# Performance work log

Measured on AMD Instinct MI355X. Metric: run time of the kernel, lower is better.

The kernel has to match this reference:

```python
import jax, jax.numpy as jnp
import numpy as np

ROW = COL = 8   # unfold tile size
KS = 5          # gaussian raster kernel size
C1 = 6          # high-freq feature split

def conv2d(x, w, b=None, pad=0):
    y = jax.lax.conv_general_dilated(x, w, (1, 1), [(pad, pad), (pad, pad)],
                                     dimension_numbers=('NCHW', 'OIHW', 'NCHW'))
    if b is not None:
        y = y + b[None, :, None, None]
    return y

def unfold_tiles(x, r, c):
    # non-overlapping Unfold(kernel=(r,c), stride=(r,c)) -> [B*L, C, r, c]
    B, C, H, W = x.shape
    x = x.reshape(B, C, H // r, r, W // c, c).transpose(0, 2, 4, 1, 3, 5)
    return x.reshape(B * (H // r) * (W // c), C, r, c)

def fold_tiles(t, B, C, H, W, r, c):
    t = t.reshape(B, H // r, W // c, C, r, c).transpose(0, 3, 1, 4, 2, 5)
    return t.reshape(B, C, H, W)

def setup_inputs() -> dict:
    key = jax.random.key(0)
    ks = jax.random.split(key, 16)
    B, NF, H, W, P = 32, 48, 128, 128, 81
    inp = {
        'ms': jax.random.normal(ks[0], (B, 4, 32, 32), jnp.float32),
        'feat': jax.random.normal(ks[1], (B, NF, H, W), jnp.float32),
        'V': jax.random.normal(ks[2], (B, NF, H, W), jnp.float32),
        'logits_raw': jax.random.normal(ks[3], (B, P, H, W), jnp.float32),
        'sigma_x': jax.random.uniform(ks[4], (P,), jnp.float32, 0.2, 3.0),
        'sigma_y': jax.random.uniform(ks[5], (P,), jnp.float32, 0.2, 3.0),
        'opacity': jax.random.uniform(ks[6], (P,), jnp.float32, 0.1, 1.0),
        'rho': jax.random.uniform(ks[7], (P,), jnp.float32, -0.9, 0.9),
        'w_v2': jax.random.normal(ks[8], (42, 42, 1, 1), jnp.float32) * 0.05,
        'w_fine': jax.random.normal(ks[9], (4, NF, 3, 3), jnp.float32) * 0.05,
        'b_fine': jax.random.normal(ks[10], (4,), jnp.float32) * 0.05,
        'w_res': jax.random.normal(ks[11], (4, NF, 1, 1), jnp.float32) * 0.05,
        'b_res': jax.random.normal(ks[12], (4,), jnp.float32) * 0.05,
    }
    return inp

def reference(ms, feat, V, logits_raw, sigma_x, sigma_y, opacity, rho,
              w_v2, w_fine, b_fine, w_res, b_res):
    B, nf, H, W = feat.shape
    # soft class assignment (gumbel_softmax tau=1, zero-noise deterministic surrogate)
    logits = jax.nn.softmax(logits_raw, axis=1)
    feat1, lr_feat = feat[:, :C1], feat[:, C1:]
    V1, V2 = V[:, :C1], V[:, C1:]
    # H,W are already multiples of ROW/COL -> bicubic-to-same-size is identity
    uf = unfold_tiles(feat1, ROW, COL)        # [B*L, c1, 8, 8]
    ul = unfold_tiles(logits, ROW, COL)       # [B*L, P, 8, 8]
    uv1 = unfold_tiles(V1, ROW, COL)          # [B*L, c1, 8, 8]
    # weighted gaussian params per in-tile position, averaged over all tiles
    pm = ul.reshape(ul.shape[0], ul.shape[1], -1).mean(axis=0)   # [P, 64]
    wsx = sigma_x @ pm; wsy = sigma_y @ pm                       # [64]
    wop = opacity @ pm; wr = rho @ pm                            # [64]
    # 2x2 covariance per point, analytic inverse
    a = wsx ** 2; bcv = wr * wsx * wsy; d = wsy ** 2
    det = a * d - bcv ** 2
    i00 = d / det; i01 = -bcv / det; i11 = a / det
    ax = jnp.linspace(-5.0, 5.0, KS)
    xx = ax[:, None]; yy = ax[None, :]
    z = -0.5 * (i00[:, None, None] * xx ** 2 + 2.0 * i01[:, None, None] * xx * yy
                + i11[:, None, None] * yy ** 2)
    kern = jnp.exp(z) / (2.0 * jnp.pi * jnp.sqrt(det))[:, None, None]   # [64, KS, KS]
    kern = kern / kern.max(axis=(-2, -1), keepdims=True)
    kern = kern * wop[:, None, None]
    # splat: place each point's kernel centered at its grid position in the 8x8 tile
    pad = KS // 2
    ii = jnp.arange(ROW * COL) // COL
    jj = jnp.arange(ROW * COL) % COL
    canvas = jnp.zeros((ROW + 2 * pad, COL + 2 * pad), kern.dtype)
    place = jax.vmap(lambda k, i, j: jax.lax.dynamic_update_slice(canvas, k, (i, j)))
    K = place(kern, ii, jj)[:, pad:pad + ROW, pad:pad + COL]             # [64, 8, 8]
    colors = uf.reshape(uf.shape[0], C1, ROW * COL)                      # [N, c1, 64]
    rendered = jnp.einsum('ncp,phw->nchw', colors, K) * uv1              # modulate by V1
    hr = fold_tiles(rendered, B, C1, H, W, ROW, COL)                     # [B, c1, H, W]
    # squeeze-style channel attention on low branch, modulated by V2
    gap = lr_feat.mean(axis=(2, 3), keepdims=True)
    attn = jax.nn.sigmoid(conv2d(gap, w_v2))
    lr_mod = lr_feat * attn * V2
    out_feat = jnp.concatenate([hr, lr_mod], axis=1)                     # [B, n_feats, H, W]
    up_ms = jax.image.resize(ms, (B, ms.shape[1], H, W), method='bilinear')
    out = conv2d(out_feat, w_fine, b_fine, pad=1) + conv2d(feat, w_res, b_res) + up_ms
    return out
```

## Files before the change

### kernel.cpp

```cpp
#include <hip/hip_runtime.h>

#define NBATCH 32
#define NFEAT 48
#define C1c 6
#define LRC 42
#define HH 128
#define WW 128
#define HWSZ 16384
#define NP 81
#define NQ 64

#define OFF_PM   0
#define OFF_GAP  5184
#define OFF_K    6528
#define OFF_ATTN 10624
#define OFF_WB   11968
#define OFF_HR   14272

__global__ __launch_bounds__(256, 2) void k_phase1(const float* __restrict__ logits,
                                                   const float* __restrict__ feat,
                                                   const float* __restrict__ ms,
                                                   const float* __restrict__ w_res,
                                                   const float* __restrict__ b_fine,
                                                   const float* __restrict__ b_res,
                                                   float* __restrict__ pm_sum,
                                                   float* __restrict__ gap,
                                                   float* __restrict__ out) {
    int bid = blockIdx.x;
    int tid = threadIdx.x;
    if (bid < 512) {
        int b   = bid >> 4;
        int ygp = (bid >> 2) & 3;
        int qq  = bid & 3;
        int x   = tid & 127;
        int yg  = ygp * 2 + (tid >> 7);
        float acc[NP];
#pragma unroll
        for (int p = 0; p < NP; ++p) acc[p] = 0.f;
        for (int k = 0; k < 4; ++k) {
            int y = yg + 8 * (qq * 4 + k);
            const float* base = logits + (size_t)b * NP * HWSZ + (y << 7) + x;
            float ev[NP];
            float s = 0.f;
#pragma unroll
            for (int p = 0; p < NP; ++p) { ev[p] = __expf(base[(size_t)p * HWSZ]); s += ev[p]; }
            float inv = 1.f / s;
#pragma unroll
            for (int p = 0; p < NP; ++p) acc[p] += ev[p] * inv;
        }
        int lane = tid & 63;
#pragma unroll
        for (int p = 0; p < NP; ++p) {
            float e = acc[p];
            e += __shfl_xor(e, 8);
            e += __shfl_xor(e, 16);
            e += __shfl_xor(e, 32);
            if (lane < 8) atomicAdd(&pm_sum[p * NQ + (yg << 3) + lane], e);
        }
    } else {
        int gid = bid - 512;
        int b     = gid >> 3;
        int strip = gid & 7;
        int row = (strip << 4) + (tid >> 4);
        int x0  = (tid & 15) << 3;
        int poff = (row << 7) + x0;
        int lane = tid & 63;
        const float* fb = feat + (((size_t)b * NFEAT) << 14);
        float a[8][4];
#pragma unroll
        for (int j = 0; j < 8; ++j)
#pragma unroll
            for (int o = 0; o < 4; ++o) a[j][o] = 0.f;
        for (int c = 0; c < NFEAT; ++c) {
            const float* fp = fb + ((size_t)c << 14) + poff;
            float4 f0 = *(const float4*)fp;
            float4 f1 = *(const float4*)(fp + 4);
            float wr0 = w_res[c], wr1 = w_res[NFEAT + c], wr2 = w_res[2 * NFEAT + c], wr3 = w_res[3 * NFEAT + c];
            float px[8] = { f0.x, f0.y, f0.z, f0.w, f1.x, f1.y, f1.z, f1.w };
#pragma unroll
            for (int j = 0; j < 8; ++j) {
                a[j][0] += wr0 * px[j]; a[j][1] += wr1 * px[j];
                a[j][2] += wr2 * px[j]; a[j][3] += wr3 * px[j];
            }
            if (c >= C1c) {
                float s = (f0.x + f0.y + f0.z + f0.w) + (f1.x + f1.y + f1.z + f1.w);
                s += __shfl_xor(s, 1);  s += __shfl_xor(s, 2);  s += __shfl_xor(s, 4);
                s += __shfl_xor(s, 8);  s += __shfl_xor(s, 16); s += __shfl_xor(s, 32);
                if (lane == 0) atomicAdd(&gap[b * LRC + (c - C1c)], s);
            }
        }
        float syf = (row + 0.5f) * 0.25f - 0.5f;
        int y0i = (int)floorf(syf); float fy = syf - (float)y0i;
        int y0c = min(31, max(0, y0i)), y1c = min(31, max(0, y0i + 1));
        float fxv[8]; int x0v[8], x1v[8];
#pragma unroll
        for (int j = 0; j < 8; ++j) {
            float sxf = (x0 + j + 0.5f) * 0.25f - 0.5f;
            int x0i = (int)floorf(sxf);
            fxv[j] = sxf - (float)x0i;
            x0v[j] = min(31, max(0, x0i));
            x1v[j] = min(31, max(0, x0i + 1));
        }
#pragma unroll
        for (int o = 0; o < 4; ++o) {
            const float* mb = ms + ((size_t)(b * 4 + o) << 10);
            float addc = b_fine[o] + b_res[o];
            float res[8];
#pragma unroll
            for (int j = 0; j < 8; ++j) {
                float m00 = mb[(y0c << 5) + x0v[j]], m01 = mb[(y0c << 5) + x1v[j]];
                float m10 = mb[(y1c << 5) + x0v[j]], m11 = mb[(y1c << 5) + x1v[j]];
                float up = (m00 * (1.f - fxv[j]) + m01 * fxv[j]) * (1.f - fy)
                         + (m10 * (1.f - fxv[j]) + m11 * fxv[j]) * fy;
                res[j] = a[j][o] + addc + up;
            }
            float* op = out + (((size_t)(b * 4 + o)) << 14) + poff;
            *(float4*)op = make_float4(res[0], res[1], res[2], res[3]);
            *(float4*)(op + 4) = make_float4(res[4], res[5], res[6], res[7]);
        }
    }
}

__global__ __launch_bounds__(256) void k_small(const float* __restrict__ pm_sum,
                                               const float* __restrict__ gap_sum,
                                               const float* __restrict__ sigx,
                                               const float* __restrict__ sigy,
                                               const float* __restrict__ opac,
                                               const float* __restrict__ rho,
                                               const float* __restrict__ w_v2,
                                               const float* __restrict__ w_fine,
                                               const float* __restrict__ w_res,
                                               float* __restrict__ Kmat,
                                               float* __restrict__ attn,
                                               float* __restrict__ wbuf) {
    int tid = threadIdx.x;
    if (tid < 64) {
        int q = tid;
        float wsx = 0.f, wsy = 0.f, wop = 0.f, wr = 0.f;
        for (int p = 0; p < NP; ++p) {
            float pv = pm_sum[p * NQ + q] * (1.f / 8192.f);
            wsx += sigx[p] * pv;
            wsy += sigy[p] * pv;
            wop += opac[p] * pv;
            wr  += rho[p]  * pv;
        }
        float a = wsx * wsx, d = wsy * wsy, bc = wr * wsx * wsy;
        float det = a * d - bc * bc;
        float i00 = d / det, i01 = -bc / det, i11 = a / det;
        int iq = q >> 3, jq = q & 7;
        for (int h = 0; h < 8; ++h)
            for (int w = 0; w < 8; ++w) {
                int ki = h - iq + 2, kj = w - jq + 2;
                float val = 0.f;
                if (ki >= 0 && ki < 5 && kj >= 0 && kj < 5) {
                    float xx = -5.f + 2.5f * ki, yy = -5.f + 2.5f * kj;
                    val = wop * __expf(-0.5f * (i00 * xx * xx + 2.f * i01 * xx * yy + i11 * yy * yy));
                }
                Kmat[(q << 6) + (h << 3) + w] = val;
            }
    }
    for (int i = tid; i < NBATCH * LRC; i += 256) {
        int b = i / LRC, co = i % LRC;
        float s = 0.f;
        for (int ci = 0; ci < LRC; ++ci) s += w_v2[co * LRC + ci] * gap_sum[b * LRC + ci];
        s *= (1.f / 16384.f);
        attn[i] = 1.f / (1.f + __expf(-s));
    }
    for (int i = tid; i < NFEAT * 48; i += 256) {
        int c = i / 48, j = i - c * 48;
        float v = 0.f;
        if (j < 36) v = w_fine[(j / 9) * (NFEAT * 9) + c * 9 + (j % 9)];
        else if (j < 40) v = w_res[(j - 36) * NFEAT + c];
        wbuf[i] = v;
    }
}

__global__ __launch_bounds__(256) void k_hr(const float* __restrict__ feat,
                                            const float* __restrict__ V,
                                            const float* __restrict__ Kmat,
                                            float* __restrict__ hrbuf) {
    __shared__ __align__(16) float lK[4096];
    __shared__ __align__(16) float lF[2 * 16 * 128];
    int bid = blockIdx.x;
    int b   = bid / 24;
    int r   = bid - b * 24;
    int strip = r / 3;
    int ch  = (r - strip * 3) * 2;
    int y0  = strip << 4;
    int tid = threadIdx.x;
    {
        const float4* ks = (const float4*)Kmat;
        float4* kd = (float4*)lK;
        for (int i = tid; i < 1024; i += 256) kd[i] = ks[i];
        float4* fd = (float4*)lF;
        const float* fb = feat + (((size_t)b * NFEAT + ch) << 14) + (y0 << 7);
        for (int i = tid; i < 1024; i += 256) {
            int c = i >> 9, rem = i & 511;
            fd[i] = *(const float4*)&fb[((size_t)c << 14) + (rem << 2)];
        }
    }
    __syncthreads();
    int tile = tid >> 3, hrow = tid & 7;
    int tr = tile >> 4, tx = tile & 15;
    float acc[2][8];
#pragma unroll
    for (int c = 0; c < 2; ++c)
#pragma unroll
        for (int j = 0; j < 8; ++j) acc[c][j] = 0.f;
    int fbase = (tr << 3) * 128 + (tx << 3);
    for (int q = 0; q < 64; ++q) {
        int iq = q >> 3, jq = q & 7;
        const float4 k0 = *(const float4*)&lK[(q << 6) + (hrow << 3)];
        const float4 k1 = *(const float4*)&lK[(q << 6) + (hrow << 3) + 4];
#pragma unroll
        for (int c = 0; c < 2; ++c) {
            float col = lF[(c << 11) + fbase + (iq << 7) + jq];
            acc[c][0] += col * k0.x; acc[c][1] += col * k0.y;
            acc[c][2] += col * k0.z; acc[c][3] += col * k0.w;
            acc[c][4] += col * k1.x; acc[c][5] += col * k1.y;
            acc[c][6] += col * k1.z; acc[c][7] += col * k1.w;
        }
    }
    int y = y0 + (tr << 3) + hrow;
#pragma unroll
    for (int c = 0; c < 2; ++c) {
        const float4* vp = (const float4*)(V + (((size_t)b * NFEAT + ch + c) << 14) + ((size_t)y << 7) + (tx << 3));
        float4 v0 = vp[0], v1 = vp[1];
        float4 r0, r1;
        r0.x = acc[c][0] * v0.x; r0.y = acc[c][1] * v0.y; r0.z = acc[c][2] * v0.z; r0.w = acc[c][3] * v0.w;
        r1.x = acc[c][4] * v1.x; r1.y = acc[c][5] * v1.y; r1.z = acc[c][6] * v1.z; r1.w = acc[c][7] * v1.w;
        float4* op = (float4*)(hrbuf + (((size_t)b * C1c + ch + c) << 14) + ((size_t)y << 7) + (tx << 3));
        op[0] = r0; op[1] = r1;
    }
}

#define CCH 8
__global__ __launch_bounds__(256, 4) void k_conv(const float* __restrict__ feat,
                                                 const float* __restrict__ V,
                                                 const float* __restrict__ wbuf,
                                                 const float* __restrict__ hrbuf,
                                                 const float* __restrict__ attn,
                                                 float* __restrict__ out) {
    __shared__ __align__(16) float s_in[CCH][18 * 40];
    int bid0 = blockIdx.x;
    int rid  = (bid0 & 7) * 128 + (bid0 >> 3);
    int b    = rid >> 5;
    int t32  = rid & 31;
    int ty0  = (t32 >> 2) << 4;
    int tx0  = (t32 & 3) << 5;
    int tid  = threadIdx.x;
    int ty   = tid >> 4;
    int tx   = tid & 15;
    int gy   = ty0 + ty;
    int gx0  = tx0 + 2 * tx;
    int own_goff = (gy << 7) + gx0;
    int own_lds  = (ty + 1) * 40 + 4 + 2 * tx;

    bool hhas = tid < 100;
    int rr, cc;
    if (tid < 34)      { rr = 0;        cc = tid; }
    else if (tid < 68) { rr = 17;       cc = tid - 34; }
    else if (tid < 84) { rr = tid - 67; cc = 0; }
    else               { rr = tid - 83; cc = 33; }
    int hsy = ty0 - 1 + rr, hsx = tx0 - 1 + cc;
    float hfm = (hsy >= 0 && hsy < HH && hsx >= 0 && hsx < WW) ? 1.f : 0.f;
    int hoff = (min(HH - 1, max(0, hsy)) << 7) + min(WW - 1, max(0, hsx));
    int hlds = rr * 40 + 3 + cc;

    float a00 = 0.f, a01 = 0.f, a02 = 0.f, a03 = 0.f;
    float a10 = 0.f, a11 = 0.f, a12 = 0.f, a13 = 0.f;

    for (int cb = 0; cb < NFEAT; cb += CCH) {
        __syncthreads();
        for (int k = 0; k < CCH; ++k) {
            int c = cb + k;
            if (c < C1c) {
                const float* hsrc = hrbuf + (((size_t)b * C1c + c) << 14);
                *(float2*)&s_in[k][own_lds] = *(const float2*)&hsrc[own_goff];
                if (hhas) s_in[k][hlds] = hsrc[hoff] * hfm;
            } else {
                float am = attn[b * LRC + (c - C1c)];
                const float* fsrc = feat + (((size_t)b * NFEAT + c) << 14);
                const float* vsrc = V    + (((size_t)b * NFEAT + c) << 14);
                float2 f2 = *(const float2*)&fsrc[own_goff];
                float2 v2 = *(const float2*)&vsrc[own_goff];
                *(float2*)&s_in[k][own_lds] = make_float2(f2.x * v2.x * am, f2.y * v2.y * am);
                if (hhas) s_in[k][hlds] = fsrc[hoff] * vsrc[hoff] * (am * hfm);
            }
        }
        __syncthreads();
        for (int k = 0; k < CCH; ++k) {
            int c = cb + k;
            const float* wc = wbuf + c * 48;
            int base = ty * 40 + 3 + 2 * tx;
            float tA0 = s_in[k][base];
            float2 m0 = *(const float2*)&s_in[k][base + 1];
            float tD0 = s_in[k][base + 3];
            float tA1 = s_in[k][base + 40];
            float2 m1 = *(const float2*)&s_in[k][base + 41];
            float tD1 = s_in[k][base + 43];
            float tA2 = s_in[k][base + 80];
            float2 m2 = *(const float2*)&s_in[k][base + 81];
            float tD2 = s_in[k][base + 83];
#pragma unroll
            for (int o = 0; o < 4; ++o) {
                float w0 = wc[o * 9 + 0], w1 = wc[o * 9 + 1], w2 = wc[o * 9 + 2];
                float w3 = wc[o * 9 + 3], w4 = wc[o * 9 + 4], w5 = wc[o * 9 + 5];
                float w6 = wc[o * 9 + 6], w7 = wc[o * 9 + 7], w8 = wc[o * 9 + 8];
                float r0 = w0 * tA0 + w1 * m0.x + w2 * m0.y
                         + w3 * tA1 + w4 * m1.x + w5 * m1.y
                         + w6 * tA2 + w7 * m2.x + w8 * m2.y;
                float r1 = w0 * m0.x + w1 * m0.y + w2 * tD0
                         + w3 * m1.x + w4 * m1.y + w5 * tD1
                         + w6 * m2.x + w7 * m2.y + w8 * tD2;
                if (o == 0) { a00 += r0; a10 += r1; }
                else if (o == 1) { a01 += r0; a11 += r1; }
                else if (o == 2) { a02 += r0; a12 += r1; }
                else { a03 += r0; a13 += r1; }
            }
        }
    }
    float ar[4][2] = { {a00, a10}, {a01, a11}, {a02, a12}, {a03, a13} };
#pragma unroll
    for (int o = 0; o < 4; ++o) {
        float* op = out + (((size_t)(b * 4 + o)) << 14) + own_goff;
        float2 base = *(const float2*)op;
        *(float2*)op = make_float2(base.x + ar[o][0], base.y + ar[o][1]);
    }
}

extern "C" void kernel_launch(void* const* d_in, const int* in_sizes, int n_in,
                              void* d_out, int out_size, void* d_ws, size_t ws_size,
                              hipStream_t stream) {
    (void)in_sizes; (void)n_in; (void)out_size; (void)ws_size;
    const float* ms     = (const float*)d_in[0];
    const float* feat   = (const float*)d_in[1];
    const float* V      = (const float*)d_in[2];
    const float* logits = (const float*)d_in[3];
    const float* sigx   = (const float*)d_in[4];
    const float* sigy   = (const float*)d_in[5];
    const float* opac   = (const float*)d_in[6];
    const float* rho    = (const float*)d_in[7];
    const float* w_v2   = (const float*)d_in[8];
    const float* w_fine = (const float*)d_in[9];
    const float* b_fine = (const float*)d_in[10];
    const float* w_res  = (const float*)d_in[11];
    const float* b_res  = (const float*)d_in[12];
    float* ws  = (float*)d_ws;
    float* out = (float*)d_out;

    hipMemsetAsync(ws + OFF_PM, 0, (size_t)(NP * NQ + NBATCH * LRC) * sizeof(float), stream);
    k_phase1<<<512 + 256, 256, 0, stream>>>(logits, feat, ms, w_res, b_fine, b_res,
                                            ws + OFF_PM, ws + OFF_GAP, out);
    k_small<<<1, 256, 0, stream>>>(ws + OFF_PM, ws + OFF_GAP, sigx, sigy, opac, rho, w_v2,
                                   w_fine, w_res, ws + OFF_K, ws + OFF_ATTN, ws + OFF_WB);
    k_hr<<<768, 256, 0, stream>>>(feat, V, ws + OFF_K, ws + OFF_HR);
    k_conv<<<1024, 256, 0, stream>>>(feat, V, ws + OFF_WB, ws + OFF_HR, ws + OFF_ATTN, out);
}
```

Measured before the change: 206.8 us.

## Split fused softmax-sum phase into two-pass softmax kernels and separate base conv kernel

Replaces the fused phase-1 kernel, whose softmax branch held 81-element accumulator arrays per thread, with three kernels. The first computes per-pixel inverse softmax denominators, the second recomputes exp per (batch, class) plane and reduces into the per-tile-position sums, and the third does the 1x1 residual conv, GAP and bilinear upsample with narrower per-thread work. The aim is to remove register pressure and the low parallelism of the old softmax branch. The cost is reading the logits twice and more launches. The out buffer is borrowed as scratch for the inverse sums before k_base overwrites it.

```diff
diff --git a/kernel.cpp b/kernel.cpp
--- a/kernel.cpp
+++ b/kernel.cpp
@@ -17,107 +17,116 @@
 #define OFF_WB   11968
 #define OFF_HR   14272
 
-__global__ __launch_bounds__(256, 2) void k_phase1(const float* __restrict__ logits,
-                                                   const float* __restrict__ feat,
-                                                   const float* __restrict__ ms,
-                                                   const float* __restrict__ w_res,
-                                                   const float* __restrict__ b_fine,
-                                                   const float* __restrict__ b_res,
-                                                   float* __restrict__ pm_sum,
-                                                   float* __restrict__ gap,
-                                                   float* __restrict__ out) {
+__global__ __launch_bounds__(256) void k_sm1(const float* __restrict__ logits,
+                                             float* __restrict__ invbuf) {
+    int idx = blockIdx.x * 256 + threadIdx.x;
+    int b   = idx >> 12;
+    int pos = (idx & 4095) << 2;
+    const float* base = logits + (((size_t)b * NP) << 14) + pos;
+    float s0 = 0.f, s1 = 0.f, s2 = 0.f, s3 = 0.f;
+    for (int p = 0; p < NP; ++p) {
+        float4 v = *(const float4*)&base[(size_t)p << 14];
+        s0 += __expf(v.x); s1 += __expf(v.y); s2 += __expf(v.z); s3 += __expf(v.w);
+    }
+    *(float4*)&invbuf[(size_t)idx << 2] =
+        make_float4(1.f / s0, 1.f / s1, 1.f / s2, 1.f / s3);
+}
+
+__global__ __launch_bounds__(256) void k_sm2(const float* __restrict__ logits,
+                                             const float* __restrict__ invbuf,
+                                             float* __restrict__ pm_sum) {
     int bid = blockIdx.x;
+    int b = bid / NP, p = bid - b * NP;
+    const float* base = logits + ((size_t)(b * NP + p) << 14);
+    const float* ib   = invbuf + ((size_t)b << 14);
     int tid = threadIdx.x;
-    if (bid < 512) {
-        int b   = bid >> 4;
-        int ygp = (bid >> 2) & 3;
-        int qq  = bid & 3;
-        int x   = tid & 127;
-        int yg  = ygp * 2 + (tid >> 7);
-        float acc[NP];
-#pragma unroll
-        for (int p = 0; p < NP; ++p) acc[p] = 0.f;
-        for (int k = 0; k < 4; ++k) {
-            int y = yg + 8 * (qq * 4 + k);
-            const float* base = logits + (size_t)b * NP * HWSZ + (y << 7) + x;
-            float ev[NP];
-            float s = 0.f;
-#pragma unroll
-            for (int p = 0; p < NP; ++p) { ev[p] = __expf(base[(size_t)p * HWSZ]); s += ev[p]; }
-            float inv = 1.f / s;
-#pragma unroll
-            for (int p = 0; p < NP; ++p) acc[p] += ev[p] * inv;
-        }
-        int lane = tid & 63;
-#pragma unroll
-        for (int p = 0; p < NP; ++p) {
-            float e = acc[p];
-            e += __shfl_xor(e, 8);
-            e += __shfl_xor(e, 16);
-            e += __shfl_xor(e, 32);
-            if (lane < 8) atomicAdd(&pm_sum[p * NQ + (yg << 3) + lane], e);
-        }
-    } else {
-        int gid = bid - 512;
-        int b     = gid >> 3;
-        int strip = gid & 7;
-        int row = (strip << 4) + (tid >> 4);
-        int x0  = (tid & 15) << 3;
-        int poff = (row << 7) + x0;
-        int lane = tid & 63;
-        const float* fb = feat + (((size_t)b * NFEAT) << 14);
-        float a[8][4];
-#pragma unroll
-        for (int j = 0; j < 8; ++j)
-#pragma unroll
-            for (int o = 0; o < 4; ++o) a[j][o] = 0.f;
-        for (int c = 0; c < NFEAT; ++c) {
-            const float* fp = fb + ((size_t)c << 14) + poff;
-            float4 f0 = *(const float4*)fp;
-            float4 f1 = *(const float4*)(fp + 4);
-            float wr0 = w_res[c], wr1 = w_res[NFEAT + c], wr2 = w_res[2 * NFEAT + c], wr3 = w_res[3 * NFEAT + c];
-            float px[8] = { f0.x, f0.y, f0.z, f0.w, f1.x, f1.y, f1.z, f1.w };
-#pragma unroll
-            for (int j = 0; j < 8; ++j) {
-                a[j][0] += wr0 * px[j]; a[j][1] += wr1 * px[j];
-                a[j][2] += wr2 * px[j]; a[j][3] += wr3 * px[j];
-            }
-            if (c >= C1c) {
-                float s = (f0.x + f0.y + f0.z + f0.w) + (f1.x + f1.y + f1.z + f1.w);
-                s += __shfl_xor(s, 1);  s += __shfl_xor(s, 2);  s += __shfl_xor(s, 4);
-                s += __shfl_xor(s, 8);  s += __shfl_xor(s, 16); s += __shfl_xor(s, 32);
-                if (lane == 0) atomicAdd(&gap[b * LRC + (c - C1c)], s);
-            }
-        }
-        float syf = (row + 0.5f) * 0.25f - 0.5f;
-        int y0i = (int)floorf(syf); float fy = syf - (float)y0i;
-        int y0c = min(31, max(0, y0i)), y1c = min(31, max(0, y0i + 1));
-        float fxv[8]; int x0v[8], x1v[8];
-#pragma unroll
-        for (int j = 0; j < 8; ++j) {
-            float sxf = (x0 + j + 0.5f) * 0.25f - 0.5f;
-            int x0i = (int)floorf(sxf);
-            fxv[j] = sxf - (float)x0i;
-            x0v[j] = min(31, max(0, x0i));
-            x1v[j] = min(31, max(0, x0i + 1));
-        }
-#pragma unroll
-        for (int o = 0; o < 4; ++o) {
-            const float* mb = ms + ((size_t)(b * 4 + o) << 10);
-            float addc = b_fine[o] + b_res[o];
-            float res[8];
-#pragma unroll
-            for (int j = 0; j < 8; ++j) {
-                float m00 = mb[(y0c << 5) + x0v[j]], m01 = mb[(y0c << 5) + x1v[j]];
-                float m10 = mb[(y1c << 5) + x0v[j]], m11 = mb[(y1c << 5) + x1v[j]];
-                float up = (m00 * (1.f - fxv[j]) + m01 * fxv[j]) * (1.f - fy)
-                         + (m10 * (1.f - fxv[j]) + m11 * fxv[j]) * fy;
-                res[j] = a[j][o] + addc + up;
-            }
-            float* op = out + (((size_t)(b * 4 + o)) << 14) + poff;
-            *(float4*)op = make_float4(res[0], res[1], res[2], res[3]);
-            *(float4*)(op + 4) = make_float4(res[4], res[5], res[6], res[7]);
-        }
+    int r0 = tid >> 5, xt = tid & 31;
+    float a0 = 0.f, a1 = 0.f, a2 = 0.f, a3 = 0.f;
+    int off = (r0 << 7) + (xt << 2);
+    for (int k = 0; k < 16; ++k, off += 1024) {
+        float4 l4 = *(const float4*)&base[off];
+        float4 i4 = *(const float4*)&ib[off];
+        a0 += __expf(l4.x) * i4.x;
+        a1 += __expf(l4.y) * i4.y;
+        a2 += __expf(l4.z) * i4.z;
+        a3 += __expf(l4.w) * i4.w;
+    }
+#pragma unroll
+    for (int m = 2; m <= 16; m <<= 1) {
+        a0 += __shfl_xor(a0, m); a1 += __shfl_xor(a1, m);
+        a2 += __shfl_xor(a2, m); a3 += __shfl_xor(a3, m);
+    }
+    if (xt < 2) {
+        int qb = p * NQ + (r0 << 3) + ((xt & 1) << 2);
+        atomicAdd(&pm_sum[qb + 0], a0);
+        atomicAdd(&pm_sum[qb + 1], a1);
+        atomicAdd(&pm_sum[qb + 2], a2);
+        atomicAdd(&pm_sum[qb + 3], a3);
+    }
+}
+
+__global__ __launch_bounds__(256) void k_base(const float* __restrict__ feat,
+                                              const float* __restrict__ ms,
+                                              const float* __restrict__ w_res,
+                                              const float* __restrict__ b_fine,
+                                              const float* __restrict__ b_res,
+                                              float* __restrict__ gap,
+                                              float* __restrict__ out) {
+    int gid = blockIdx.x;
+    int b = gid >> 4, strip = gid & 15;
+    int tid = threadIdx.x;
+    int row = (strip << 3) + (tid >> 5);
+    int x0  = (tid & 31) << 2;
+    int poff = (row << 7) + x0;
+    int lane = tid & 63;
+    const float* fb = feat + (((size_t)b * NFEAT) << 14);
+    float a[4][4];
+#pragma unroll
+    for (int j = 0; j < 4; ++j)
+#pragma unroll
+        for (int o = 0; o < 4; ++o) a[j][o] = 0.f;
+    for (int c = 0; c < NFEAT; ++c) {
+        float4 f = *(const float4*)&fb[((size_t)c << 14) + poff];
+        float wr0 = w_res[c], wr1 = w_res[NFEAT + c];
+        float wr2 = w_res[2 * NFEAT + c], wr3 = w_res[3 * NFEAT + c];
+        a[0][0] += wr0 * f.x; a[0][1] += wr1 * f.x; a[0][2] += wr2 * f.x; a[0][3] += wr3 * f.x;
+        a[1][0] += wr0 * f.y; a[1][1] += wr1 * f.y; a[1][2] += wr2 * f.y; a[1][3] += wr3 * f.y;
+        a[2][0] += wr0 * f.z; a[2][1] += wr1 * f.z; a[2][2] += wr2 * f.z; a[2][3] += wr3 * f.z;
+        a[3][0] += wr0 * f.w; a[3][1] += wr1 * f.w; a[3][2] += wr2 * f.w; a[3][3] += wr3 * f.w;
+        if (c >= C1c) {
+            float s = (f.x + f.y) + (f.z + f.w);
+            s += __shfl_xor(s, 1);  s += __shfl_xor(s, 2);  s += __shfl_xor(s, 4);
+            s += __shfl_xor(s, 8);  s += __shfl_xor(s, 16); s += __shfl_xor(s, 32);
+            if (lane == 0) atomicAdd(&gap[b * LRC + (c - C1c)], s);
+        }
+    }
+    float syf = (row + 0.5f) * 0.25f - 0.5f;
+    int y0i = (int)floorf(syf); float fy = syf - (float)y0i;
+    int y0c = min(31, max(0, y0i)), y1c = min(31, max(0, y0i + 1));
+    float fxv[4]; int x0v[4], x1v[4];
+#pragma unroll
+    for (int j = 0; j < 4; ++j) {
+        float sxf = (x0 + j + 0.5f) * 0.25f - 0.5f;
+        int x0i = (int)floorf(sxf);
+        fxv[j] = sxf - (float)x0i;
+        x0v[j] = min(31, max(0, x0i));
+        x1v[j] = min(31, max(0, x0i + 1));
+    }
+#pragma unroll
+    for (int o = 0; o < 4; ++o) {
+        const float* mb = ms + ((size_t)(b * 4 + o) << 10);
+        float addc = b_fine[o] + b_res[o];
+        float res[4];
+#pragma unroll
+        for (int j = 0; j < 4; ++j) {
+            float m00 = mb[(y0c << 5) + x0v[j]], m01 = mb[(y0c << 5) + x1v[j]];
+            float m10 = mb[(y1c << 5) + x0v[j]], m11 = mb[(y1c << 5) + x1v[j]];
+            float up = (m00 * (1.f - fxv[j]) + m01 * fxv[j]) * (1.f - fy)
+                     + (m10 * (1.f - fxv[j]) + m11 * fxv[j]) * fy;
+            res[j] = a[j][o] + addc + up;
+        }
+        *(float4*)&out[(((size_t)(b * 4 + o)) << 14) + poff] =
+            make_float4(res[0], res[1], res[2], res[3]);
     }
 }
 
@@ -350,8 +359,9 @@
     float* out = (float*)d_out;
 
     hipMemsetAsync(ws + OFF_PM, 0, (size_t)(NP * NQ + NBATCH * LRC) * sizeof(float), stream);
-    k_phase1<<<512 + 256, 256, 0, stream>>>(logits, feat, ms, w_res, b_fine, b_res,
-                                            ws + OFF_PM, ws + OFF_GAP, out);
+    k_sm1<<<512, 256, 0, stream>>>(logits, out);
+    k_sm2<<<NBATCH * NP, 256, 0, stream>>>(logits, out, ws + OFF_PM);
+    k_base<<<512, 256, 0, stream>>>(feat, ms, w_res, b_fine, b_res, ws + OFF_GAP, out);
     k_small<<<1, 256, 0, stream>>>(ws + OFF_PM, ws + OFF_GAP, sigx, sigy, opac, rho, w_v2,
                                    w_fine, w_res, ws + OFF_K, ws + OFF_ATTN, ws + OFF_WB);
     k_hr<<<768, 256, 0, stream>>>(feat, V, ws + OFF_K, ws + OFF_HR);
```

Result: slower. 242.7 us (+17.4%).
